# Performance work log

Hardware: AMD Instinct MI355X
Metric: run time of the kernel (lower is better)

Reference implementation:

```python
import jax, jax.numpy as jnp
import numpy as np

B, S, H = 4, 4096, 2048
CIN, COUT, K, G = 4096, 4096, 4, 8


def setup_inputs() -> dict:
    key = jax.random.key(0)
    ks = jax.random.split(key, 7)
    sc = 0.02
    return {
        "x": jax.random.normal(ks[0], (B, S, H), dtype=jnp.float32),
        "W_in": jax.random.normal(ks[1], (CIN, H), dtype=jnp.float32) * sc,
        "b_in": jax.random.normal(ks[2], (CIN,), dtype=jnp.float32) * sc,
        "conv_w": jax.random.normal(ks[3], (COUT, CIN // G, K), dtype=jnp.float32) * sc,
        "conv_b": jax.random.normal(ks[4], (COUT,), dtype=jnp.float32) * sc,
        "W_out": jax.random.normal(ks[5], (H, COUT), dtype=jnp.float32) * sc,
        "b_out": jax.random.normal(ks[6], (H,), dtype=jnp.float32) * sc,
    }


def reference(x, W_in, b_in, conv_w, conv_b, W_out, b_out):
    # input projection: [B,S,H] -> [B,S,CIN]
    h = jnp.einsum("bsh,ch->bsc", x, W_in) + b_in
    # causal grouped conv1d over sequence dim: NCW layout
    h = h.transpose(0, 2, 1)  # [B, CIN, S]
    k = conv_w.shape[2]
    groups = h.shape[1] // conv_w.shape[1]
    y = jax.lax.conv_general_dilated(
        h, conv_w,
        window_strides=(1,),
        padding=[(k - 1, 0)],  # left-pad only == pad k-1 then trim trailing
        feature_group_count=groups,
        dimension_numbers=("NCH", "OIH", "NCH"),
    )  # [B, COUT, S]
    y = jax.nn.silu(y + conv_b[None, :, None])
    y = y.transpose(0, 2, 1)  # [B, S, COUT]
    # output projection: [B,S,COUT] -> [B,S,H]
    out = jnp.einsum("bsc,hc->bsh", y, W_out) + b_out
    return out
```

## Files before the change

kernel.cpp:

```cpp
#include <hip/hip_runtime.h>
#include <cstdint>
#include <cstddef>

static constexpr int Bn   = 4;
static constexpr int Sn   = 4096;
static constexpr int Hn   = 2048;
static constexpr int CINn = 4096;
static constexpr int COUTn= 4096;
static constexpr int GCn  = 512;
static constexpr int Kt   = 4;
static constexpr int Mn   = Bn * Sn;
static constexpr int SPn  = Sn + 3;

typedef _Float16 half8 __attribute__((ext_vector_type(8)));
typedef _Float16 half4 __attribute__((ext_vector_type(4)));
typedef float    floatx4 __attribute__((ext_vector_type(4)));


__global__ void cvt_f32_f16(const float* __restrict__ src, _Float16* __restrict__ dst, int n4) {
    int i = blockIdx.x * blockDim.x + threadIdx.x;
    if (i < n4) {
        float4 v = ((const float4*)src)[i];
        half4 h;
        h[0] = (_Float16)v.x; h[1] = (_Float16)v.y;
        h[2] = (_Float16)v.z; h[3] = (_Float16)v.w;
        ((half4*)dst)[i] = h;
    }
}

__global__ void cvt_convw(const float* __restrict__ src, _Float16* __restrict__ dst) {
    int t = blockIdx.x * blockDim.x + threadIdx.x;
    int co = t >> 9, ci = t & 511;
    float4 v = ((const float4*)src)[(co << 9) + ci];
    size_t base = (size_t)co * 2048 + ci;
    dst[base]        = (_Float16)v.x;
    dst[base + 512]  = (_Float16)v.y;
    dst[base + 1024] = (_Float16)v.z;
    dst[base + 1536] = (_Float16)v.w;
}

__global__ void zero_pads(_Float16* __restrict__ Hp) {
    int t = blockIdx.x * blockDim.x + threadIdx.x;
    int b = t / (3 * CINn);
    int off = t - b * (3 * CINn);
    Hp[(size_t)b * SPn * CINn + off] = (_Float16)0.f;
}


__device__ __forceinline__ void async16(const void* g, void* l) {
    __builtin_amdgcn_global_load_lds(
        (__attribute__((address_space(1))) void*)(g),
        (__attribute__((address_space(3))) void*)(l),
        16, 0, 0);
}

#define BAR()  __builtin_amdgcn_s_barrier()
#define SB0()  __builtin_amdgcn_sched_barrier(0)
#define WL0()  asm volatile("s_waitcnt lgkmcnt(0)" ::: "memory")
#define WV(n)  asm volatile("s_waitcnt vmcnt(" #n ")" ::: "memory")
#define PRIO1() __builtin_amdgcn_s_setprio(1)
#define PRIO0() __builtin_amdgcn_s_setprio(0)

template <int MODE>
__global__ __launch_bounds__(512, 2) void gemm8(
    const _Float16* __restrict__ A,
    const _Float16* __restrict__ Bw,
    const float* __restrict__ bias,
    void* __restrict__ outp,
    int Kd, int Ntiles)
{
    __shared__ __align__(16) _Float16 smem[2][2][256 * 64];

    const int t  = threadIdx.x;
    const int w  = t >> 6;
    const int l  = t & 63;
    const int wm = w >> 2;
    const int wn = w & 3;

    const int nwg = (int)gridDim.x;
    const int bid = (int)blockIdx.x;
    const int swz = (bid & 7) * (nwg >> 3) + (bid >> 3);
    const int mt = swz / Ntiles, nt = swz - mt * Ntiles;
    const int m0 = mt * 256, n0 = nt * 256;

    const int sr  = t >> 3;
    const int scb = ((t & 7) ^ (sr & 7)) << 3;
    const _Float16* pa0;
    if (MODE == 1) {
        const int ma = m0 + sr;
        pa0 = A + ((size_t)((ma >> 12) * SPn + (ma & 4095)) << 12) + (n0 >> 9) * 512 + scb;
    } else {
        pa0 = A + (size_t)(m0 + sr) * Kd + scb;
    }
    const _Float16* pb0 = Bw + (size_t)(n0 + sr) * Kd + scb;
    const size_t aq = (MODE == 1) ? (size_t)(64 * 4096) : (size_t)64 * Kd;
    const size_t bq = (size_t)64 * Kd;
    const int wst = w * 512;

    const int fr = l & 15, quad = l >> 4, sw = fr & 7;

    floatx4 acc[8][4] = {};
    half8 afA[4][2];
    half8 afB[4][2];
    half8 bf[4][2];

    const int NT = Kd >> 6;

#define KADJ(kk) ((MODE == 1) ? ((kk) + (((kk) >> 9) * 3584)) : (kk))
#define STA(b, q, ko) async16(pa0 + (size_t)(q) * aq + (ko), &smem[b][0][(q) * 4096 + wst])
#define STB(b, q, ko) async16(pb0 + (size_t)(q) * bq + (ko), &smem[b][1][(q) * 4096 + wst])

#define LCOL(ks) ((((ks << 2) + quad) ^ sw) << 3)

#define RD_B0(cb) do { \
    _Pragma("unroll") for (int nf = 0; nf < 2; ++nf) \
    _Pragma("unroll") for (int ks = 0; ks < 2; ++ks) { \
        int row = wn * 64 + nf * 16 + fr; \
        bf[nf][ks] = *(const half8*)(&smem[cb][1][row * 64 + LCOL(ks)]); \
    } } while (0)

#define RD_B1(cb) do { \
    _Pragma("unroll") for (int nf = 0; nf < 2; ++nf) \
    _Pragma("unroll") for (int ks = 0; ks < 2; ++ks) { \
        int row = wn * 64 + 32 + nf * 16 + fr; \
        bf[2 + nf][ks] = *(const half8*)(&smem[cb][1][row * 64 + LCOL(ks)]); \
    } } while (0)

#define RD_A1(cb) do { \
    _Pragma("unroll") for (int mf = 0; mf < 4; ++mf) \
    _Pragma("unroll") for (int ks = 0; ks < 2; ++ks) { \
        int row = wm * 128 + 64 + mf * 16 + fr; \
        afB[mf][ks] = *(const half8*)(&smem[cb][0][row * 64 + LCOL(ks)]); \
    } } while (0)

#define RD_A0_LO(cb) do { \
    _Pragma("unroll") for (int mf = 0; mf < 2; ++mf) \
    _Pragma("unroll") for (int ks = 0; ks < 2; ++ks) { \
        int row = wm * 128 + mf * 16 + fr; \
        afA[mf][ks] = *(const half8*)(&smem[cb][0][row * 64 + LCOL(ks)]); \
    } } while (0)

#define RD_A0_HI(cb) do { \
    _Pragma("unroll") for (int mf = 2; mf < 4; ++mf) \
    _Pragma("unroll") for (int ks = 0; ks < 2; ++ks) { \
        int row = wm * 128 + mf * 16 + fr; \
        afA[mf][ks] = *(const half8*)(&smem[cb][0][row * 64 + LCOL(ks)]); \
    } } while (0)

#define MMA_PH(AF, mh, nh) do { \
    _Pragma("unroll") for (int mf = 0; mf < 4; ++mf) \
    _Pragma("unroll") for (int nf = 0; nf < 2; ++nf) \
    _Pragma("unroll") for (int ks = 0; ks < 2; ++ks) \
        acc[(mh) * 4 + mf][(nh) * 2 + nf] = __builtin_amdgcn_mfma_f32_16x16x32_f16( \
            AF[mf][ks], bf[(nh) * 2 + nf][ks], acc[(mh) * 4 + mf][(nh) * 2 + nf], 0, 0, 0); \
    } while (0)

    {
        STA(0, 0, 0); STA(0, 1, 0); STA(0, 2, 0); STA(0, 3, 0);
        STB(0, 0, 0); STB(0, 1, 0); STB(0, 2, 0); STB(0, 3, 0);
        const int ka1 = KADJ(64);
        STA(1, 0, ka1); STA(1, 1, ka1); STA(1, 2, ka1); STA(1, 3, ka1);
        STB(1, 0, 64); STB(1, 1, 64); STB(1, 2, 64); STB(1, 3, 64);
        WV(0); BAR(); SB0();
        RD_A0_LO(0); RD_A0_HI(0); RD_B0(0);
    }

    PRIO1();
    for (int tt = 0; tt < NT; ++tt) {
        const int cur = tt & 1, nxt = cur ^ 1;
        const bool s1 = (tt + 1 < NT), s2 = (tt + 2 < NT);
        const int ka2 = KADJ((tt + 2) << 6);
        const int kb2 = (tt + 2) << 6;

        RD_B1(cur);
        MMA_PH(afA, 0, 0);
        PRIO0(); WL0(); BAR(); SB0(); PRIO1();
        if (s2) { STA(cur, 0, ka2); STA(cur, 2, ka2);
                  STB(cur, 0, kb2); STB(cur, 1, kb2); STB(cur, 2, kb2); STB(cur, 3, kb2); }

        RD_A1(cur);
        MMA_PH(afA, 0, 1);
        PRIO0();
        if (s2) { WV(6); } else { WV(0); }
        WL0(); BAR(); SB0(); PRIO1();
        if (s2) { STA(cur, 1, ka2); STA(cur, 3, ka2); }

        if (s1) RD_A0_LO(nxt);
        MMA_PH(afB, 1, 0);

        if (s1) { RD_A0_HI(nxt); RD_B0(nxt); }
        MMA_PH(afB, 1, 1);
    }
    PRIO0();

    #pragma unroll
    for (int nf = 0; nf < 4; ++nf) {
        const int ncol = n0 + wn * 64 + nf * 16 + fr;
        const float bv = bias[ncol];
        #pragma unroll
        for (int mf = 0; mf < 8; ++mf) {
            const int mb = m0 + wm * 128 + mf * 16 + quad * 4;
            #pragma unroll
            for (int r = 0; r < 4; ++r) {
                const int m = mb + r;
                float v = acc[mf][nf][r] + bv;
                if (MODE == 0) {
                    const size_t row = (size_t)((m >> 12) * SPn + 3 + (m & 4095));
                    ((_Float16*)outp)[(row << 12) + ncol] = (_Float16)v;
                } else if (MODE == 1) {
                    v = v * (1.0f / (1.0f + __expf(-v)));
                    ((_Float16*)outp)[((size_t)m << 12) + ncol] = (_Float16)v;
                } else {
                    ((float*)outp)[((size_t)m << 11) + ncol] = v;
                }
            }
        }
    }
#undef KADJ
#undef STA
#undef STB
#undef LCOL
#undef RD_B0
#undef RD_B1
#undef RD_A1
#undef RD_A0_LO
#undef RD_A0_HI
#undef MMA_PH
}


extern "C" void kernel_launch(void* const* d_in, const int* in_sizes, int n_in,
                              void* d_out, int out_size, void* d_ws, size_t ws_size,
                              hipStream_t stream) {
    const float* x      = (const float*)d_in[0];
    const float* W_in   = (const float*)d_in[1];
    const float* b_in   = (const float*)d_in[2];
    const float* conv_w = (const float*)d_in[3];
    const float* conv_b = (const float*)d_in[4];
    const float* W_out  = (const float*)d_in[5];
    const float* b_out  = (const float*)d_in[6];
    float* out = (float*)d_out;

    char* ws = (char*)d_ws;
    _Float16* Xh  = (_Float16*)(ws);
    _Float16* W1h = (_Float16*)(ws + 67108864);
    _Float16* Wch = (_Float16*)(ws + 83886080);
    _Float16* W2h = (_Float16*)(ws + 100663296);
    _Float16* Hp  = (_Float16*)(ws + 117440512);
    _Float16* Yh  = (_Float16*)(ws + 251756544);
    (void)ws_size; (void)in_sizes; (void)n_in; (void)out_size;

    cvt_f32_f16<<<32768, 256, 0, stream>>>(x,     Xh,  Mn * Hn / 4);
    cvt_f32_f16<<<8192,  256, 0, stream>>>(W_in,  W1h, CINn * Hn / 4);
    cvt_convw <<<8192,  256, 0, stream>>>(conv_w, Wch);
    cvt_f32_f16<<<8192,  256, 0, stream>>>(W_out, W2h, Hn * COUTn / 4);
    zero_pads <<<192,   256, 0, stream>>>(Hp);

    gemm8<0><<<(Mn / 256) * (CINn / 256), 512, 0, stream>>>(Xh, W1h, b_in, (void*)Hp, Hn, CINn / 256);
    gemm8<1><<<(Mn / 256) * (COUTn / 256), 512, 0, stream>>>(Hp, Wch, conv_b, (void*)Yh, GCn * Kt, COUTn / 256);
    gemm8<2><<<(Mn / 256) * (Hn / 256), 512, 0, stream>>>(Yh, W2h, b_out, (void*)out, COUTn, Hn / 256);
}
```

Measured before the change: 1.049 ms.

## Restructure GEMM main loop into 8-phase barrier-interleaved schedule with per-quarter pointers

The GEMM main loop is unrolled by two K-tiles and split into eight phases. Each phase issues LDS fragment reads and a slice of async global-to-LDS loads, then synchronises with barriers around an MFMA block, in the style of the hipBLASLt/HipKittens 8-wave ping-pong schedule. Global pointers for each 64-row quarter are precomputed, replacing the base-plus-stride arithmetic. The aim is to spread memory traffic evenly across phases and keep the two co-resident workgroups alternating on the matrix units. The cost is many more barriers per iteration, the loss of register prefetch of the next tile's fragments, and the assumption that NT is even.

```diff
diff --git a/kernel.cpp b/kernel.cpp
--- a/kernel.cpp
+++ b/kernel.cpp
@@ -57,6 +57,7 @@
 #define BAR()  __builtin_amdgcn_s_barrier()
 #define SB0()  __builtin_amdgcn_sched_barrier(0)
 #define WL0()  asm volatile("s_waitcnt lgkmcnt(0)" ::: "memory")
+#define WL8()  asm volatile("s_waitcnt lgkmcnt(8)" ::: "memory")
 #define WV(n)  asm volatile("s_waitcnt vmcnt(" #n ")" ::: "memory")
 #define PRIO1() __builtin_amdgcn_s_setprio(1)
 #define PRIO0() __builtin_amdgcn_s_setprio(0)
@@ -85,16 +86,18 @@
 
     const int sr  = t >> 3;
     const int scb = ((t & 7) ^ (sr & 7)) << 3;
-    const _Float16* pa0;
-    if (MODE == 1) {
-        const int ma = m0 + sr;
-        pa0 = A + ((size_t)((ma >> 12) * SPn + (ma & 4095)) << 12) + (n0 >> 9) * 512 + scb;
-    } else {
-        pa0 = A + (size_t)(m0 + sr) * Kd + scb;
-    }
-    const _Float16* pb0 = Bw + (size_t)(n0 + sr) * Kd + scb;
-    const size_t aq = (MODE == 1) ? (size_t)(64 * 4096) : (size_t)64 * Kd;
-    const size_t bq = (size_t)64 * Kd;
+    const _Float16* pa[4];
+    const _Float16* pb[4];
+    #pragma unroll
+    for (int q = 0; q < 4; ++q) {
+        const int ma = m0 + q * 64 + sr;
+        if (MODE == 1) {
+            pa[q] = A + ((size_t)((ma >> 12) * SPn + (ma & 4095)) << 12) + (n0 >> 9) * 512 + scb;
+        } else {
+            pa[q] = A + (size_t)ma * Kd + scb;
+        }
+        pb[q] = Bw + (size_t)(n0 + q * 64 + sr) * Kd + scb;
+    }
     const int wst = w * 512;
 
     const int fr = l & 15, quad = l >> 4, sw = fr & 7;
@@ -105,46 +108,40 @@
     half8 bf[4][2];
 
     const int NT = Kd >> 6;
+    const int NITER = NT >> 1;
 
 #define KADJ(kk) ((MODE == 1) ? ((kk) + (((kk) >> 9) * 3584)) : (kk))
-#define STA(b, q, ko) async16(pa0 + (size_t)(q) * aq + (ko), &smem[b][0][(q) * 4096 + wst])
-#define STB(b, q, ko) async16(pb0 + (size_t)(q) * bq + (ko), &smem[b][1][(q) * 4096 + wst])
+#define STA(b, q, ko) async16(pa[q] + (ko), &smem[b][0][(q) * 4096 + wst])
+#define STB(b, q, ko) async16(pb[q] + (ko), &smem[b][1][(q) * 4096 + wst])
 
 #define LCOL(ks) ((((ks << 2) + quad) ^ sw) << 3)
 
-#define RD_B0(cb) do { \
+#define RD_A_H0(cb) do { \
+    _Pragma("unroll") for (int mf = 0; mf < 4; ++mf) \
+    _Pragma("unroll") for (int ks = 0; ks < 2; ++ks) { \
+        int row = wm * 128 + mf * 16 + fr; \
+        afA[mf][ks] = *(const half8*)(&smem[cb][0][row * 64 + LCOL(ks)]); \
+    } } while (0)
+
+#define RD_A_H1(cb) do { \
+    _Pragma("unroll") for (int mf = 0; mf < 4; ++mf) \
+    _Pragma("unroll") for (int ks = 0; ks < 2; ++ks) { \
+        int row = wm * 128 + 64 + mf * 16 + fr; \
+        afB[mf][ks] = *(const half8*)(&smem[cb][0][row * 64 + LCOL(ks)]); \
+    } } while (0)
+
+#define RD_B_Q0(cb) do { \
     _Pragma("unroll") for (int nf = 0; nf < 2; ++nf) \
     _Pragma("unroll") for (int ks = 0; ks < 2; ++ks) { \
         int row = wn * 64 + nf * 16 + fr; \
         bf[nf][ks] = *(const half8*)(&smem[cb][1][row * 64 + LCOL(ks)]); \
     } } while (0)
 
-#define RD_B1(cb) do { \
+#define RD_B_Q1(cb) do { \
     _Pragma("unroll") for (int nf = 0; nf < 2; ++nf) \
     _Pragma("unroll") for (int ks = 0; ks < 2; ++ks) { \
         int row = wn * 64 + 32 + nf * 16 + fr; \
         bf[2 + nf][ks] = *(const half8*)(&smem[cb][1][row * 64 + LCOL(ks)]); \
-    } } while (0)
-
-#define RD_A1(cb) do { \
-    _Pragma("unroll") for (int mf = 0; mf < 4; ++mf) \
-    _Pragma("unroll") for (int ks = 0; ks < 2; ++ks) { \
-        int row = wm * 128 + 64 + mf * 16 + fr; \
-        afB[mf][ks] = *(const half8*)(&smem[cb][0][row * 64 + LCOL(ks)]); \
-    } } while (0)
-
-#define RD_A0_LO(cb) do { \
-    _Pragma("unroll") for (int mf = 0; mf < 2; ++mf) \
-    _Pragma("unroll") for (int ks = 0; ks < 2; ++ks) { \
-        int row = wm * 128 + mf * 16 + fr; \
-        afA[mf][ks] = *(const half8*)(&smem[cb][0][row * 64 + LCOL(ks)]); \
-    } } while (0)
-
-#define RD_A0_HI(cb) do { \
-    _Pragma("unroll") for (int mf = 2; mf < 4; ++mf) \
-    _Pragma("unroll") for (int ks = 0; ks < 2; ++ks) { \
-        int row = wm * 128 + mf * 16 + fr; \
-        afA[mf][ks] = *(const half8*)(&smem[cb][0][row * 64 + LCOL(ks)]); \
     } } while (0)
 
 #define MMA_PH(AF, mh, nh) do { \
@@ -161,37 +158,70 @@
         const int ka1 = KADJ(64);
         STA(1, 0, ka1); STA(1, 1, ka1); STA(1, 2, ka1); STA(1, 3, ka1);
         STB(1, 0, 64); STB(1, 1, 64); STB(1, 2, 64); STB(1, 3, 64);
-        WV(0); BAR(); SB0();
-        RD_A0_LO(0); RD_A0_HI(0); RD_B0(0);
-    }
-
-    PRIO1();
-    for (int tt = 0; tt < NT; ++tt) {
-        const int cur = tt & 1, nxt = cur ^ 1;
-        const bool s1 = (tt + 1 < NT), s2 = (tt + 2 < NT);
-        const int ka2 = KADJ((tt + 2) << 6);
-        const int kb2 = (tt + 2) << 6;
-
-        RD_B1(cur);
-        MMA_PH(afA, 0, 0);
-        PRIO0(); WL0(); BAR(); SB0(); PRIO1();
-        if (s2) { STA(cur, 0, ka2); STA(cur, 2, ka2);
-                  STB(cur, 0, kb2); STB(cur, 1, kb2); STB(cur, 2, kb2); STB(cur, 3, kb2); }
-
-        RD_A1(cur);
-        MMA_PH(afA, 0, 1);
-        PRIO0();
-        if (s2) { WV(6); } else { WV(0); }
-        WL0(); BAR(); SB0(); PRIO1();
-        if (s2) { STA(cur, 1, ka2); STA(cur, 3, ka2); }
-
-        if (s1) RD_A0_LO(nxt);
-        MMA_PH(afB, 1, 0);
-
-        if (s1) { RD_A0_HI(nxt); RD_B0(nxt); }
-        MMA_PH(afB, 1, 1);
-    }
-    PRIO0();
+        WV(0); BAR();
+    }
+
+    for (int it = 0; it < NITER; ++it) {
+        const int T = it << 1;
+        const bool s2 = (T + 2 < NT);
+        const bool s3 = (T + 3 < NT);
+        const bool lastit = (it == NITER - 1);
+        const int ka2 = KADJ((T + 2) << 6), kb2 = (T + 2) << 6;
+        const int ka3 = KADJ((T + 3) << 6), kb3 = (T + 3) << 6;
+
+        RD_A_H0(0); RD_B_Q0(0);
+        WL8(); SB0(); BAR();
+        WL0(); SB0();
+        PRIO1(); MMA_PH(afA, 0, 0); PRIO0();
+        BAR();
+
+        RD_B_Q1(0);
+        if (s2) { STA(0, 0, ka2); STA(0, 2, ka2); }
+        SB0(); BAR();
+        WL0(); SB0();
+        PRIO1(); MMA_PH(afA, 0, 1); PRIO0();
+        BAR();
+
+        RD_A_H1(0);
+        if (s2) { STB(0, 0, kb2); STB(0, 1, kb2); }
+        SB0(); BAR();
+        WL0(); SB0();
+        PRIO1(); MMA_PH(afB, 1, 0); PRIO0();
+        BAR();
+
+        if (s2) { STA(0, 1, ka2); STA(0, 3, ka2); }
+        SB0(); BAR();
+        PRIO1(); MMA_PH(afB, 1, 1); PRIO0();
+        if (lastit) { WV(0); } else { WV(6); }
+        BAR();
+
+        RD_A_H0(1); RD_B_Q0(1);
+        if (s2) { STB(0, 2, kb2); STB(0, 3, kb2); }
+        WL8(); SB0(); BAR();
+        WL0(); SB0();
+        PRIO1(); MMA_PH(afA, 0, 0); PRIO0();
+        BAR();
+
+        RD_B_Q1(1);
+        if (s3) { STA(1, 0, ka3); STA(1, 2, ka3); }
+        SB0(); BAR();
+        WL0(); SB0();
+        PRIO1(); MMA_PH(afA, 0, 1); PRIO0();
+        BAR();
+
+        RD_A_H1(1);
+        if (s3) { STB(1, 0, kb3); STB(1, 1, kb3); STB(1, 2, kb3); STB(1, 3, kb3); }
+        SB0(); BAR();
+        WL0(); SB0();
+        PRIO1(); MMA_PH(afB, 1, 0); PRIO0();
+        BAR();
+
+        if (s3) { STA(1, 1, ka3); STA(1, 3, ka3); }
+        SB0(); BAR();
+        PRIO1(); MMA_PH(afB, 1, 1); PRIO0();
+        if (lastit) { WV(0); } else { WV(6); }
+        BAR();
+    }
 
     #pragma unroll
     for (int nf = 0; nf < 4; ++nf) {
@@ -220,11 +250,10 @@
 #undef STA
 #undef STB
 #undef LCOL
-#undef RD_B0
-#undef RD_B1
-#undef RD_A1
-#undef RD_A0_LO
-#undef RD_A0_HI
+#undef RD_A_H0
+#undef RD_A_H1
+#undef RD_B_Q0
+#undef RD_B_Q1
 #undef MMA_PH
 }
 
```

After: 1.082 ms. +3.1%, slower.
